# Performance work log

Measured on AMD Instinct MI355X. Metric: run time of the kernel, lower is better.

## Reference

```python
import jax, jax.numpy as jnp
import numpy as np

H = 10          # heads
DIMS = [4, 256, 256, 256, 256, 256, 256, 2]  # model_param
B = 32768
OBS_X, OBS_Y, R = 0.0, 7.0, 4.0
L1, L2 = 3.0, 3.0


def _linear_params(key, din, dout, n=H):
    kw, kb = jax.random.split(key)
    s = 1.0 / np.sqrt(din)
    W = jax.random.uniform(kw, (n, dout, din), jnp.float32, -s, s)
    b = jax.random.uniform(kb, (n, dout), jnp.float32, -s, s)
    return W, b


def setup_inputs() -> dict:
    key = jax.random.key(0)
    ks = jax.random.split(key, 16)
    inp = {
        "x": jax.random.normal(ks[0], (B, DIMS[0]), jnp.float32),
        "sgn": 1,
        "wt": jnp.ones((H,), jnp.float32),
        "mean": jnp.zeros((DIMS[0],), jnp.float32),
        "std": jnp.ones((DIMS[0],), jnp.float32),
        "mean_label": jnp.zeros((DIMS[7],), jnp.float32),
        "std_label": jnp.ones((DIMS[7],), jnp.float32),
    }
    inp["W1"], inp["b1"] = _linear_params(ks[1], DIMS[0], DIMS[1])
    inp["W2"], inp["b2"] = _linear_params(ks[2], DIMS[1], DIMS[2])
    inp["W31"], inp["b31"] = _linear_params(ks[3], DIMS[2], DIMS[3])
    inp["W32"], inp["b32"] = _linear_params(ks[4], DIMS[2], DIMS[4])
    inp["W41"], inp["b41"] = _linear_params(ks[5], DIMS[3], DIMS[5])
    inp["W42"], inp["b42"] = _linear_params(ks[6], DIMS[4], DIMS[6])
    inp["W51"], inp["b51"] = _linear_params(ks[7], DIMS[5], DIMS[7])
    inp["W52"], inp["b52"] = _linear_params(ks[8], DIMS[6], DIMS[7])
    return inp


def _forward(x, W1, b1, W2, b2, W31, b31, W32, b32, W41, b41, W42, b42,
             W51, b51, W52, b52, wt, mean, std, mean_label, std_label):
    relu = jax.nn.relu
    x0 = x * std + mean                                   # de-normalized state [B,4]

    # Stacked per-head MLP (heads axis h)
    x1 = relu(jnp.einsum('bi,hoi->hbo', x, W1) + b1[:, None, :])
    x2 = relu(jnp.einsum('hbi,hoi->hbo', x1, W2) + b2[:, None, :])
    x31 = relu(jnp.einsum('hbi,hoi->hbo', x2, W31) + b31[:, None, :])
    x32 = relu(jnp.einsum('hbi,hoi->hbo', x2, W32) + b32[:, None, :])
    x41 = relu(jnp.einsum('hbi,hoi->hbo', x31, W41) + b41[:, None, :])
    x42 = relu(jnp.einsum('hbi,hoi->hbo', x32, W42) + b42[:, None, :])
    x51 = jnp.einsum('hbi,hoi->hbo', x41, W51) + b51[:, None, :]       # [H,B,2] QP linear cost
    x52 = 4.0 * jax.nn.sigmoid(jnp.einsum('hbi,hoi->hbo', x42, W52) + b52[:, None, :])  # [H,B,2] CBF gains

    # CBF geometric quantities (shared across heads)
    t1, w1, t2, w2 = x0[:, 0], x0[:, 1], x0[:, 2], x0[:, 3]
    s1, s2, c1, c2 = jnp.sin(t1), jnp.sin(t2), jnp.cos(t1), jnp.cos(t2)
    px = L1 * c1 + L2 * c2 - OBS_X
    py = L1 * s1 + L2 * s2 - OBS_Y
    vx = -L1 * s1 * w1 - L2 * s2 * w2
    vy = L1 * c1 * w1 + L2 * c2 * w2
    barrier = px ** 2 + py ** 2 - R ** 2
    b_dot = 2 * px * vx + 2 * py * vy
    Lf2b = (2 * vx ** 2 + 2 * vy ** 2
            + 2 * px * (-L1 * c1 * w1 ** 2 - L2 * c2 * w2 ** 2)
            + 2 * py * (-L1 * s1 * w1 ** 2 - L2 * s2 * w2 ** 2))
    LgLfbu1 = 2 * px * (-L1 * s1) + 2 * py * (L1 * c1)
    LgLfbu2 = 2 * px * (-L2 * s2) + 2 * py * (L2 * c2)
    g = jnp.stack([-LgLfbu1, -LgLfbu2], axis=-1)          # [B,2] constraint row

    # h uses head-0's x52[:,0] for every head (self.x52 caching in the torch code)
    a0 = x52[0, :, 0]                                     # [B]
    b_i = x52[:, :, 1]                                    # [H,B]
    h = Lf2b[None] + (a0[None] + b_i) * b_dot[None] + a0[None] * b_i * barrier[None]  # [H,B]

    # QP min 0.5 u'u + p'u  s.t. g.u <= h  -> closed-form halfspace projection
    u_unc = -x51                                          # [H,B,2]
    gg = jnp.sum(g * g, axis=-1)                          # [B]
    viol = jnp.einsum('hbc,bc->hb', u_unc, g) - h         # [H,B]
    lam = jnp.maximum(viol, 0.0) / gg[None]               # active-set multiplier
    u = u_unc - lam[..., None] * g[None]                  # [H,B,2]
    u = (u - mean_label) / std_label

    w = jax.nn.softmax(wt)                                # exp(wt)/sum(exp(wt))
    return jnp.einsum('h,hbc->bc', w, u)                  # [B,2]


def reference(x, sgn, wt, mean, std, mean_label, std_label,
              W1, b1, W2, b2, W31, b31, W32, b32, W41, b41, W42, b42,
              W51, b51, W52, b52):
    return _forward(x, W1, b1, W2, b2, W31, b31, W32, b32, W41, b41,
                    W42, b42, W51, b51, W52, b52, wt, mean, std,
                    mean_label, std_label)
```

## Files before the change

### kernel.cpp

```cpp
#include <hip/hip_runtime.h>
#include <hip/hip_bf16.h>

typedef __attribute__((ext_vector_type(8)))  short bf16x8_t;
typedef __attribute__((ext_vector_type(16))) float f32x16_t;
typedef __attribute__((ext_vector_type(4)))  float f32x4_t;

#define HN 10
#define BN 32768
#define DH 256
#define MT 64

#define KS17 17
#define HE17   (KS17*8*64*8)
#define ARRE17 (HN*HE17)

#define OFF_A     0
#define OFF_S5    32768
#define SMEM_BYTES 33280

#define MFMA32 __builtin_amdgcn_mfma_f32_32x32x16_bf16

#define BAR_LDS() asm volatile("s_waitcnt lgkmcnt(0)\ns_barrier" ::: "memory")

__device__ __forceinline__ unsigned swzoff(int row, int colb) {
  return (unsigned)(row * 512 + (colb ^ ((row & 31) << 4)));
}

__device__ __forceinline__ unsigned short f2bf(float v) {
  __hip_bfloat16 hb = __float2bfloat16(v);
  return *reinterpret_cast<unsigned short*>(&hb);
}
__device__ __forceinline__ unsigned pk2bf(float lo, float hi_) {
  return (unsigned)f2bf(lo) | ((unsigned)f2bf(hi_) << 16);
}

struct WPtrs { const float* w[5]; const float* b[5]; };

extern "C" __global__ void pack_big(WPtrs p, unsigned short* __restrict__ dst)
{
  int g = blockIdx.x * blockDim.x + threadIdx.x;
  if (g >= 5 * HN * KS17 * 8 * 64) return;
  int lane = g & 63; int t = g >> 6;
  int nt = t & 7; t >>= 3;
  int ks = t % KS17; t /= KS17;
  int h = t % HN;
  int a = t / HN;
  int col = nt * 32 + (lane & 31);
  int hi = lane >> 5;
  unsigned short* d = dst + (size_t)a * ARRE17 + (size_t)h * HE17
                    + ((ks * 8 + nt) * 64 + lane) * 8;
  if (ks < 16) {
    const float* src = p.w[a] + (size_t)h * 65536 + col * 256 + ks * 16 + hi * 8;
    #pragma unroll
    for (int j = 0; j < 8; ++j) d[j] = f2bf(src[j]);
  } else {
    float bv = p.b[a][(size_t)h * 256 + col];
    #pragma unroll
    for (int j = 0; j < 8; ++j) d[j] = (hi == 0 && j == 0) ? f2bf(bv) : (unsigned short)0;
  }
}

extern "C" __global__ void pack_w5(const float* __restrict__ w51, const float* __restrict__ w52,
                                   const float* __restrict__ b51, const float* __restrict__ b52,
                                   unsigned short* __restrict__ dst)
{
  int g = blockIdx.x * blockDim.x + threadIdx.x;
  if (g >= 2 * HN * KS17 * 64) return;
  int lane = g & 63; int t = g >> 6;
  int ks = t % KS17; t /= KS17;
  int h = t % HN;
  int br = t / HN;
  const float* w = br ? w52 : w51;
  const float* b = br ? b52 : b51;
  int col = lane & 31;
  int hi = lane >> 5;
  unsigned short* d = dst + ((size_t)(br * HN + h) * KS17 + ks) * 512 + lane * 8;
  if (ks < 16) {
    int k = ks * 16 + hi * 8;
    #pragma unroll
    for (int j = 0; j < 8; ++j) {
      float v = (col < 2) ? w[(size_t)h * 512 + col * 256 + k + j] : 0.f;
      d[j] = f2bf(v);
    }
  } else {
    float bv = (col < 2) ? b[(size_t)h * 2 + col] : 0.f;
    #pragma unroll
    for (int j = 0; j < 8; ++j) d[j] = (hi == 0 && j == 0) ? f2bf(bv) : (unsigned short)0;
  }
}

extern "C" __global__ void pack_w1(const float* __restrict__ w1, const float* __restrict__ b1,
                                   unsigned short* __restrict__ dst)
{
  int g = blockIdx.x * blockDim.x + threadIdx.x;
  if (g >= HN * 8 * 64) return;
  int lane = g & 63; int t = g >> 6;
  int nt = t & 7;
  int h = t >> 3;
  int col = nt * 32 + (lane & 31);
  int hi = lane >> 5;
  unsigned short* d = dst + (size_t)h * 4096 + ((size_t)nt * 64 + lane) * 8;
  #pragma unroll
  for (int j = 0; j < 8; ++j) {
    int k = hi * 8 + j;
    float v = 0.f;
    if (k < 4)       v = w1[(size_t)h * 1024 + col * 4 + k];
    else if (k == 4) v = b1[(size_t)h * 256 + col];
    d[j] = f2bf(v);
  }
}


template<bool SAVE>
__device__ __forceinline__ void write_actT(char* sout, const f32x16_t acc[2][2],
                                           unsigned sv[2][2][8], int lane, int wave)
{
  const int r31 = lane & 31, hi = lane >> 5;
  #pragma unroll
  for (int mt = 0; mt < 2; ++mt) {
    const int row = mt * 32 + r31;
    #pragma unroll
    for (int nt = 0; nt < 2; ++nt) {
      #pragma unroll
      for (int g = 0; g < 4; ++g) {
        const int col0 = (wave * 2 + nt) * 32 + 8 * g + 4 * hi;
        unsigned w0 = pk2bf(fmaxf(acc[mt][nt][4 * g + 0], 0.f),
                            fmaxf(acc[mt][nt][4 * g + 1], 0.f));
        unsigned w1 = pk2bf(fmaxf(acc[mt][nt][4 * g + 2], 0.f),
                            fmaxf(acc[mt][nt][4 * g + 3], 0.f));
        if (SAVE) { sv[mt][nt][2 * g] = w0; sv[mt][nt][2 * g + 1] = w1; }
        unsigned long long pk = (unsigned long long)w0 | ((unsigned long long)w1 << 32);
        *(unsigned long long*)(sout + swzoff(row, col0 * 2)) = pk;
      }
    }
  }
}

template<bool SAVE>
__device__ __forceinline__ void gemm_ip(char* buf, const char* wb,
                                        unsigned sv[2][2][8],
                                        int lane, int wave, bf16x8_t ones)
{
  const int r31 = lane & 31, hi = lane >> 5;
  f32x16_t acc[2][2];
  #pragma unroll
  for (int mt = 0; mt < 2; ++mt)
    #pragma unroll
    for (int nt = 0; nt < 2; ++nt)
      #pragma unroll
      for (int i = 0; i < 16; ++i) acc[mt][nt][i] = 0.f;

  bf16x8_t c0[2], c1[2], c2[2];
  #pragma unroll
  for (int nt = 0; nt < 2; ++nt) {
    c0[nt] = *(const bf16x8_t*)(wb + nt * 1024);
    c1[nt] = *(const bf16x8_t*)(wb + 8192 + nt * 1024);
  }
  #pragma unroll
  for (int ks = 0; ks < KS17; ++ks) {
    if (ks < KS17 - 2) {
      #pragma unroll
      for (int nt = 0; nt < 2; ++nt)
        c2[nt] = *(const bf16x8_t*)(wb + (ks + 2) * 8192 + nt * 1024);
    }
    bf16x8_t a[2];
    #pragma unroll
    for (int mt = 0; mt < 2; ++mt)
      a[mt] = (ks < 16)
        ? *(const bf16x8_t*)(buf + swzoff(mt * 32 + r31, ks * 32 + hi * 16))
        : ones;
    #pragma unroll
    for (int mt = 0; mt < 2; ++mt) {
      acc[mt][0] = MFMA32(c0[0], a[mt], acc[mt][0], 0, 0, 0);
      acc[mt][1] = MFMA32(c0[1], a[mt], acc[mt][1], 0, 0, 0);
    }
    #pragma unroll
    for (int nt = 0; nt < 2; ++nt) { c0[nt] = c1[nt]; c1[nt] = c2[nt]; }
  }
  BAR_LDS();
  write_actT<SAVE>(buf, acc, sv, lane, wave);
  BAR_LDS();
}

__device__ __forceinline__ void final_pp(const char* sin, float* s5,
                                         const unsigned short* __restrict__ w5,
                                         float* __restrict__ wsout,
                                         int row0, int tid, int lane, int wave,
                                         bf16x8_t ones)
{
  const int r31 = lane & 31, hi = lane >> 5;
  if (wave < 2) {
    const int mt = wave;
    f32x16_t acc;
    #pragma unroll
    for (int i = 0; i < 16; ++i) acc[i] = 0.f;
    #pragma unroll
    for (int ks = 0; ks < KS17; ++ks) {
      bf16x8_t a = (ks < 16)
        ? *(const bf16x8_t*)(sin + swzoff(mt * 32 + r31, ks * 32 + hi * 16))
        : ones;
      bf16x8_t b = *(const bf16x8_t*)(w5 + (size_t)(ks * 64 + lane) * 8);
      acc = MFMA32(a, b, acc, 0, 0, 0);
    }
    if (r31 < 2) {
      #pragma unroll
      for (int r = 0; r < 16; ++r) {
        int row = mt * 32 + (r & 3) + 8 * (r >> 2) + 4 * hi;
        s5[row * 2 + r31] = acc[r];
      }
    }
  }
  BAR_LDS();
  if (tid < 128) {
    int row = tid >> 1, c = tid & 1;
    wsout[(size_t)(row0 + row) * 2 + c] = s5[row * 2 + c];
  }
}

extern "C" __global__ __launch_bounds__(256, 3)
void abnet_main(const float* __restrict__ x,
                const unsigned short* __restrict__ wpk,
                const unsigned short* __restrict__ w5pk,
                const unsigned short* __restrict__ w1pk,
                float* __restrict__ ws51, float* __restrict__ ws52)
{
  extern __shared__ char smem[];
  char*  bufA = smem + OFF_A;
  float* s5   = (float*)(smem + OFF_S5);

  const int tid  = threadIdx.x;
  const int lane = tid & 63, wave = tid >> 6;
  const int L  = (blockIdx.x & 7) * 640 + (blockIdx.x >> 3);
  const int rt = L & 511;
  const int h  = L >> 9;
  const int row0 = rt * MT;

  const int r31 = lane & 31, hi = lane >> 5;

  bf16x8_t ones;
  #pragma unroll
  for (int j = 0; j < 8; ++j) ones[j] = 0;
  if (hi == 0) ones[0] = (short)0x3F80;

  const size_t woff = (size_t)(wave * 2) * 1024 + (size_t)lane * 16;
  const char* W2w  = (const char*)(wpk + (size_t)h * HE17) + woff;
  const char* W31w = (const char*)(wpk + 1 * (size_t)ARRE17 + (size_t)h * HE17) + woff;
  const char* W32w = (const char*)(wpk + 2 * (size_t)ARRE17 + (size_t)h * HE17) + woff;
  const char* W41w = (const char*)(wpk + 3 * (size_t)ARRE17 + (size_t)h * HE17) + woff;
  const char* W42w = (const char*)(wpk + 4 * (size_t)ARRE17 + (size_t)h * HE17) + woff;

  unsigned sv[2][2][8];

  {
    const char* w1b = (const char*)(w1pk + (size_t)h * 4096) + woff;
    bf16x8_t wf[2];
    #pragma unroll
    for (int nt = 0; nt < 2; ++nt) wf[nt] = *(const bf16x8_t*)(w1b + nt * 1024);
    f32x16_t acc[2][2];
    #pragma unroll
    for (int mt = 0; mt < 2; ++mt)
      #pragma unroll
      for (int nt = 0; nt < 2; ++nt)
        #pragma unroll
        for (int i = 0; i < 16; ++i) acc[mt][nt][i] = 0.f;
    #pragma unroll
    for (int mt = 0; mt < 2; ++mt) {
      int row = row0 + mt * 32 + r31;
      f32x4_t xv = *(const f32x4_t*)(x + (size_t)row * 4);
      bf16x8_t af;
      #pragma unroll
      for (int j = 0; j < 8; ++j) {
        short v = 0;
        if (hi == 0) {
          if (j < 4)       v = (short)f2bf(xv[j]);
          else if (j == 4) v = (short)0x3F80;
        }
        af[j] = v;
      }
      acc[mt][0] = MFMA32(wf[0], af, acc[mt][0], 0, 0, 0);
      acc[mt][1] = MFMA32(wf[1], af, acc[mt][1], 0, 0, 0);
    }
    write_actT<false>(bufA, acc, sv, lane, wave);
    BAR_LDS();
  }

  gemm_ip<true >(bufA, W2w,  sv, lane, wave, ones);

  gemm_ip<false>(bufA, W31w, sv, lane, wave, ones);
  gemm_ip<false>(bufA, W41w, sv, lane, wave, ones);
  final_pp(bufA, s5, w5pk + (size_t)h * (KS17 * 512),
           ws51 + (size_t)h * BN * 2, row0, tid, lane, wave, ones);

  {
    #pragma unroll
    for (int mt = 0; mt < 2; ++mt) {
      const int row = mt * 32 + r31;
      #pragma unroll
      for (int nt = 0; nt < 2; ++nt) {
        #pragma unroll
        for (int g = 0; g < 4; ++g) {
          const int col0 = (wave * 2 + nt) * 32 + 8 * g + 4 * hi;
          unsigned long long pk = (unsigned long long)sv[mt][nt][2 * g]
                                | ((unsigned long long)sv[mt][nt][2 * g + 1] << 32);
          *(unsigned long long*)(bufA + swzoff(row, col0 * 2)) = pk;
        }
      }
    }
    BAR_LDS();
  }

  gemm_ip<false>(bufA, W32w, sv, lane, wave, ones);
  gemm_ip<false>(bufA, W42w, sv, lane, wave, ones);
  final_pp(bufA, s5, w5pk + (size_t)(HN + h) * (KS17 * 512),
           ws52 + (size_t)h * BN * 2, row0, tid, lane, wave, ones);
}

extern "C" __global__ __launch_bounds__(256)
void abnet_epi(const float* __restrict__ x, const float* __restrict__ wt,
               const float* __restrict__ mean, const float* __restrict__ stdv,
               const float* __restrict__ mlab, const float* __restrict__ slab,
               const float* __restrict__ ws51, const float* __restrict__ ws52,
               float* __restrict__ out)
{
  const int row = blockIdx.x * 256 + threadIdx.x;
  f32x4_t xr = *(const f32x4_t*)(x + (size_t)row * 4);
  float t1  = xr[0] * stdv[0] + mean[0];
  float w1v = xr[1] * stdv[1] + mean[1];
  float t2  = xr[2] * stdv[2] + mean[2];
  float w2v = xr[3] * stdv[3] + mean[3];
  float s1, c1, s2, c2;
  sincosf(t1, &s1, &c1);
  sincosf(t2, &s2, &c2);
  float px = 3.f * c1 + 3.f * c2;
  float py = 3.f * s1 + 3.f * s2 - 7.f;
  float vx = -3.f * s1 * w1v - 3.f * s2 * w2v;
  float vy =  3.f * c1 * w1v + 3.f * c2 * w2v;
  float e_bar  = px * px + py * py - 16.f;
  float e_bdot = 2.f * (px * vx + py * vy);
  float e_lf2b = 2.f * vx * vx + 2.f * vy * vy
               + 2.f * px * (-3.f * c1 * w1v * w1v - 3.f * c2 * w2v * w2v)
               + 2.f * py * (-3.f * s1 * w1v * w1v - 3.f * s2 * w2v * w2v);
  float e_g1 = 6.f * (px * s1 - py * c1);
  float e_g2 = 6.f * (px * s2 - py * c2);
  float e_ggi = 1.f / (e_g1 * e_g1 + e_g2 * e_g2);

  float m = wt[0];
  for (int i = 1; i < HN; ++i) m = fmaxf(m, wt[i]);
  float s = 0.f;
  for (int i = 0; i < HN; ++i) s += __expf(wt[i] - m);
  float sm_inv = 1.f / s;
  float ml0 = mlab[0], ml1 = mlab[1];
  float isl0 = 1.f / slab[0], isl1 = 1.f / slab[1];

  float a0r = 4.f / (1.f + __expf(-ws52[(size_t)row * 2 + 0]));
  float accu0 = 0.f, accu1 = 0.f;
  for (int h = 0; h < HN; ++h) {
    float u1 = -ws51[((size_t)h * BN + row) * 2 + 0];
    float u2 = -ws51[((size_t)h * BN + row) * 2 + 1];
    float bi = 4.f / (1.f + __expf(-ws52[((size_t)h * BN + row) * 2 + 1]));
    float hv   = e_lf2b + (a0r + bi) * e_bdot + a0r * bi * e_bar;
    float viol = u1 * e_g1 + u2 * e_g2 - hv;
    float lam  = fmaxf(viol, 0.f) * e_ggi;
    float uu1 = u1 - lam * e_g1;
    float uu2 = u2 - lam * e_g2;
    float whv = __expf(wt[h] - m) * sm_inv;
    accu0 += whv * (uu1 - ml0) * isl0;
    accu1 += whv * (uu2 - ml1) * isl1;
  }
  float2 o; o.x = accu0; o.y = accu1;
  *(float2*)(out + (size_t)row * 2) = o;
}

extern "C" void kernel_launch(void* const* d_in, const int* in_sizes, int n_in,
                              void* d_out, int out_size, void* d_ws, size_t ws_size,
                              hipStream_t stream)
{
  const float* x    = (const float*)d_in[0];
  const float* wt   = (const float*)d_in[2];
  const float* mean = (const float*)d_in[3];
  const float* stdv = (const float*)d_in[4];
  const float* mlab = (const float*)d_in[5];
  const float* slab = (const float*)d_in[6];
  const float* W1   = (const float*)d_in[7];
  const float* b1   = (const float*)d_in[8];
  WPtrs wp;
  wp.w[0] = (const float*)d_in[9];
  wp.w[1] = (const float*)d_in[11];
  wp.w[2] = (const float*)d_in[13];
  wp.w[3] = (const float*)d_in[15];
  wp.w[4] = (const float*)d_in[17];
  wp.b[0] = (const float*)d_in[10];
  wp.b[1] = (const float*)d_in[12];
  wp.b[2] = (const float*)d_in[14];
  wp.b[3] = (const float*)d_in[16];
  wp.b[4] = (const float*)d_in[18];
  const float* W51 = (const float*)d_in[19];
  const float* b51 = (const float*)d_in[20];
  const float* W52 = (const float*)d_in[21];
  const float* b52 = (const float*)d_in[22];

  char* wsb = (char*)d_ws;
  unsigned short* wpk  = (unsigned short*)wsb;
  unsigned short* w5pk = (unsigned short*)(wsb + 6963200);
  unsigned short* w1pk = (unsigned short*)(wsb + 7311360);
  float* ws51 = (float*)(wsb + 7393280);
  float* ws52 = (float*)(wsb + 10014720);

  hipLaunchKernelGGL(pack_big, dim3(1700), dim3(256), 0, stream, wp, wpk);
  hipLaunchKernelGGL(pack_w5,  dim3(85),   dim3(256), 0, stream, W51, W52, b51, b52, w5pk);
  hipLaunchKernelGGL(pack_w1,  dim3(20),   dim3(256), 0, stream, W1, b1, w1pk);

  (void)hipFuncSetAttribute(reinterpret_cast<const void*>(abnet_main),
                            hipFuncAttributeMaxDynamicSharedMemorySize, SMEM_BYTES);
  hipLaunchKernelGGL(abnet_main, dim3(512 * HN), dim3(256), SMEM_BYTES, stream,
                     x, wpk, w5pk, w1pk, ws51, ws52);
  hipLaunchKernelGGL(abnet_epi, dim3(BN / 256), dim3(256), 0, stream,
                     x, wt, mean, stdv, mlab, slab, ws51, ws52, (float*)d_out);
}
```

Before: 250.8 us.

## Fuse final 256->2 layer into register accumulators across all waves

The final output layer is now computed directly from the previous GEMM's register accumulators. Lane swaps (v_permlane32_swap) reshape the accumulators into MFMA A-operands, so the activation no longer goes through an LDS write, barrier and reread. All four waves now each do a K-slice of the final layer instead of two waves doing the full reduction, and partial sums are combined through LDS. The saved layer-2 activation restore is also folded into the first fused final, dropping a barrier. This costs a little more LDS (s5 grows to four slices), and correctness depends on the permlane register layout matching the packed W5 layout.

```diff
diff --git a/kernel.cpp b/kernel.cpp
--- a/kernel.cpp
+++ b/kernel.cpp
@@ -16,7 +16,7 @@
 
 #define OFF_A     0
 #define OFF_S5    32768
-#define SMEM_BYTES 33280
+#define SMEM_BYTES 34816
 
 #define MFMA32 __builtin_amdgcn_mfma_f32_32x32x16_bf16
 
@@ -136,13 +136,11 @@
   }
 }
 
-template<bool SAVE>
-__device__ __forceinline__ void gemm_ip(char* buf, const char* wb,
-                                        unsigned sv[2][2][8],
-                                        int lane, int wave, bf16x8_t ones)
+__device__ __forceinline__ void gemm_acc(const char* buf, const char* wb,
+                                         f32x16_t acc[2][2],
+                                         int lane, int wave, bf16x8_t ones)
 {
   const int r31 = lane & 31, hi = lane >> 5;
-  f32x16_t acc[2][2];
   #pragma unroll
   for (int mt = 0; mt < 2; ++mt)
     #pragma unroll
@@ -177,43 +175,84 @@
     #pragma unroll
     for (int nt = 0; nt < 2; ++nt) { c0[nt] = c1[nt]; c1[nt] = c2[nt]; }
   }
-  BAR_LDS();
-  write_actT<SAVE>(buf, acc, sv, lane, wave);
-  BAR_LDS();
-}
-
-__device__ __forceinline__ void final_pp(const char* sin, float* s5,
-                                         const unsigned short* __restrict__ w5,
-                                         float* __restrict__ wsout,
-                                         int row0, int tid, int lane, int wave,
-                                         bf16x8_t ones)
+}
+
+template<bool RESTORE>
+__device__ __forceinline__ void fused_final(f32x16_t acc[2][2], unsigned sv[2][2][8],
+                                            const unsigned short* __restrict__ w5,
+                                            float* s5, float* __restrict__ wsout,
+                                            char* bufA, int row0, int tid,
+                                            int lane, int wave, bf16x8_t ones)
 {
   const int r31 = lane & 31, hi = lane >> 5;
-  if (wave < 2) {
-    const int mt = wave;
-    f32x16_t acc;
-    #pragma unroll
-    for (int i = 0; i < 16; ++i) acc[i] = 0.f;
-    #pragma unroll
-    for (int ks = 0; ks < KS17; ++ks) {
-      bf16x8_t a = (ks < 16)
-        ? *(const bf16x8_t*)(sin + swzoff(mt * 32 + r31, ks * 32 + hi * 16))
-        : ones;
-      bf16x8_t b = *(const bf16x8_t*)(w5 + (size_t)(ks * 64 + lane) * 8);
-      acc = MFMA32(a, b, acc, 0, 0, 0);
-    }
-    if (r31 < 2) {
+  bf16x8_t bf[4];
+  #pragma unroll
+  for (int s = 0; s < 4; ++s)
+    bf[s] = *(const bf16x8_t*)(w5 + (size_t)((wave * 4 + s) * 64 + lane) * 8);
+  bf16x8_t bbias;
+  if (wave == 0) bbias = *(const bf16x8_t*)(w5 + (size_t)(16 * 64 + lane) * 8);
+
+  f32x16_t p[2];
+  #pragma unroll
+  for (int i = 0; i < 16; ++i) { p[0][i] = 0.f; p[1][i] = 0.f; }
+
+  #pragma unroll
+  for (int mt = 0; mt < 2; ++mt) {
+    #pragma unroll
+    for (int nt = 0; nt < 2; ++nt) {
+      #pragma unroll
+      for (int sh = 0; sh < 2; ++sh) {
+        unsigned w0 = pk2bf(fmaxf(acc[mt][nt][8 * sh + 0], 0.f),
+                            fmaxf(acc[mt][nt][8 * sh + 1], 0.f));
+        unsigned w1 = pk2bf(fmaxf(acc[mt][nt][8 * sh + 2], 0.f),
+                            fmaxf(acc[mt][nt][8 * sh + 3], 0.f));
+        unsigned v0 = pk2bf(fmaxf(acc[mt][nt][8 * sh + 4], 0.f),
+                            fmaxf(acc[mt][nt][8 * sh + 5], 0.f));
+        unsigned v1 = pk2bf(fmaxf(acc[mt][nt][8 * sh + 6], 0.f),
+                            fmaxf(acc[mt][nt][8 * sh + 7], 0.f));
+        asm("v_permlane32_swap_b32 %0, %1" : "+v"(w0), "+v"(v0));
+        asm("v_permlane32_swap_b32 %0, %1" : "+v"(w1), "+v"(v1));
+        union { unsigned u[4]; bf16x8_t f; } afu;
+        afu.u[0] = w0; afu.u[1] = w1; afu.u[2] = v0; afu.u[3] = v1;
+        p[mt] = MFMA32(afu.f, bf[nt * 2 + sh], p[mt], 0, 0, 0);
+      }
+    }
+  }
+  if (wave == 0) {
+    p[0] = MFMA32(ones, bbias, p[0], 0, 0, 0);
+    p[1] = MFMA32(ones, bbias, p[1], 0, 0, 0);
+  }
+
+  if (RESTORE) {
+    #pragma unroll
+    for (int mt = 0; mt < 2; ++mt) {
+      const int row = mt * 32 + r31;
+      #pragma unroll
+      for (int nt = 0; nt < 2; ++nt) {
+        #pragma unroll
+        for (int g = 0; g < 4; ++g) {
+          const int col0 = (wave * 2 + nt) * 32 + 8 * g + 4 * hi;
+          unsigned long long pk = (unsigned long long)sv[mt][nt][2 * g]
+                                | ((unsigned long long)sv[mt][nt][2 * g + 1] << 32);
+          *(unsigned long long*)(bufA + swzoff(row, col0 * 2)) = pk;
+        }
+      }
+    }
+  }
+
+  if (r31 < 2) {
+    #pragma unroll
+    for (int mt = 0; mt < 2; ++mt)
       #pragma unroll
       for (int r = 0; r < 16; ++r) {
         int row = mt * 32 + (r & 3) + 8 * (r >> 2) + 4 * hi;
-        s5[row * 2 + r31] = acc[r];
+        s5[wave * 128 + row * 2 + r31] = p[mt][r];
       }
-    }
   }
   BAR_LDS();
   if (tid < 128) {
-    int row = tid >> 1, c = tid & 1;
-    wsout[(size_t)(row0 + row) * 2 + c] = s5[row * 2 + c];
+    float sum = s5[tid] + s5[128 + tid] + s5[256 + tid] + s5[384 + tid];
+    wsout[(size_t)(row0 + (tid >> 1)) * 2 + (tid & 1)] = sum;
   }
 }
 
@@ -250,13 +289,13 @@
   const char* W42w = (const char*)(wpk + 4 * (size_t)ARRE17 + (size_t)h * HE17) + woff;
 
   unsigned sv[2][2][8];
+  f32x16_t acc[2][2];
 
   {
     const char* w1b = (const char*)(w1pk + (size_t)h * 4096) + woff;
     bf16x8_t wf[2];
     #pragma unroll
     for (int nt = 0; nt < 2; ++nt) wf[nt] = *(const bf16x8_t*)(w1b + nt * 1024);
-    f32x16_t acc[2][2];
     #pragma unroll
     for (int mt = 0; mt < 2; ++mt)
       #pragma unroll
@@ -284,35 +323,29 @@
     BAR_LDS();
   }
 
-  gemm_ip<true >(bufA, W2w,  sv, lane, wave, ones);
-
-  gemm_ip<false>(bufA, W31w, sv, lane, wave, ones);
-  gemm_ip<false>(bufA, W41w, sv, lane, wave, ones);
-  final_pp(bufA, s5, w5pk + (size_t)h * (KS17 * 512),
-           ws51 + (size_t)h * BN * 2, row0, tid, lane, wave, ones);
-
-  {
-    #pragma unroll
-    for (int mt = 0; mt < 2; ++mt) {
-      const int row = mt * 32 + r31;
-      #pragma unroll
-      for (int nt = 0; nt < 2; ++nt) {
-        #pragma unroll
-        for (int g = 0; g < 4; ++g) {
-          const int col0 = (wave * 2 + nt) * 32 + 8 * g + 4 * hi;
-          unsigned long long pk = (unsigned long long)sv[mt][nt][2 * g]
-                                | ((unsigned long long)sv[mt][nt][2 * g + 1] << 32);
-          *(unsigned long long*)(bufA + swzoff(row, col0 * 2)) = pk;
-        }
-      }
-    }
-    BAR_LDS();
-  }
-
-  gemm_ip<false>(bufA, W32w, sv, lane, wave, ones);
-  gemm_ip<false>(bufA, W42w, sv, lane, wave, ones);
-  final_pp(bufA, s5, w5pk + (size_t)(HN + h) * (KS17 * 512),
-           ws52 + (size_t)h * BN * 2, row0, tid, lane, wave, ones);
+  gemm_acc(bufA, W2w, acc, lane, wave, ones);
+  BAR_LDS();
+  write_actT<true>(bufA, acc, sv, lane, wave);
+  BAR_LDS();
+
+  gemm_acc(bufA, W31w, acc, lane, wave, ones);
+  BAR_LDS();
+  write_actT<false>(bufA, acc, sv, lane, wave);
+  BAR_LDS();
+
+  gemm_acc(bufA, W41w, acc, lane, wave, ones);
+  BAR_LDS();
+  fused_final<true>(acc, sv, w5pk + (size_t)h * (KS17 * 512), s5,
+                    ws51 + (size_t)h * BN * 2, bufA, row0, tid, lane, wave, ones);
+
+  gemm_acc(bufA, W32w, acc, lane, wave, ones);
+  BAR_LDS();
+  write_actT<false>(bufA, acc, sv, lane, wave);
+  BAR_LDS();
+
+  gemm_acc(bufA, W42w, acc, lane, wave, ones);
+  fused_final<false>(acc, sv, w5pk + (size_t)(HN + h) * (KS17 * 512), s5,
+                     ws52 + (size_t)h * BN * 2, bufA, row0, tid, lane, wave, ones);
 }
 
 extern "C" __global__ __launch_bounds__(256)
```

New measurement: 241.8 us (median of 2 runs). 3.6% less time.
